# Performance work log

Measured on AMD Instinct MI355X. Metric: run time of the kernel, lower is better.

Reference implementation:

```python
import jax, jax.numpy as jnp
import numpy as np

N = 50000
E = 800000


def gcn_conv(x, row, col, dinv_sqrt, W, b, n_nodes):
    # PyG GCNConv: x' = lin(x); out[col] += norm * x'[row]; out += bias
    # norm = dinv_sqrt[row] * dinv_sqrt[col] (self-loops already in row/col)
    xw = x @ W                                  # [N, out_dim]
    norm = dinv_sqrt[row] * dinv_sqrt[col]      # [E']
    msg = xw[row] * norm[:, None]               # [E', out_dim]
    out = jax.ops.segment_sum(msg, col, num_segments=n_nodes)
    return out + b


def setup_inputs() -> dict:
    key = jax.random.key(0)
    k1, k2, k3, k4 = jax.random.split(key, 4)
    x = jax.random.normal(k1, (N, 128), dtype=jnp.float32)
    edge_index = jax.random.randint(k2, (2, E), 0, N, dtype=jnp.int64)
    W1 = jax.random.normal(k3, (128, 64), dtype=jnp.float32) * (1.0 / np.sqrt(128))
    b1 = jnp.zeros((64,), dtype=jnp.float32)
    W2 = jax.random.normal(k4, (64, 32), dtype=jnp.float32) * (1.0 / np.sqrt(64))
    b2 = jnp.zeros((32,), dtype=jnp.float32)
    return {"x": x, "edge_index": edge_index, "W1": W1, "b1": b1, "W2": W2, "b2": b2}


def reference(x, edge_index, W1, b1, W2, b2):
    n_nodes = x.shape[0]
    # add self loops (fixed size -> jit friendly)
    loops = jnp.arange(n_nodes, dtype=edge_index.dtype)
    row = jnp.concatenate([edge_index[0], loops])  # source
    col = jnp.concatenate([edge_index[1], loops])  # target
    # symmetric normalization from in-degree (all edge weights = 1)
    deg = jax.ops.segment_sum(jnp.ones_like(col, dtype=x.dtype), col, num_segments=n_nodes)
    dinv_sqrt = jnp.where(deg > 0, jax.lax.rsqrt(deg), 0.0)

    h = gcn_conv(x, row, col, dinv_sqrt, W1, b1, n_nodes)
    h = jax.nn.relu(h)
    h = gcn_conv(h, row, col, dinv_sqrt, W2, b2, n_nodes)
    return jax.nn.log_softmax(h, axis=1)
```

## Files before the change

kernel.cpp:

```cpp
#include <hip/hip_runtime.h>

#define F0 128
#define F1 64
#define F2 32
#define CPB 256
#define EPB 4096

typedef unsigned short ushort_t;
typedef unsigned int uint_t;

__device__ __forceinline__ ushort_t f2bf(float f) {
    uint_t u = __float_as_uint(f);
    return (ushort_t)((u + 0x7FFFu + ((u >> 16) & 1u)) >> 16);
}
__device__ __forceinline__ float bf2f(ushort_t u) {
    return __uint_as_float((uint_t)u << 16);
}
__device__ __forceinline__ float bflo(uint_t v) { return __uint_as_float(v << 16); }
__device__ __forceinline__ float bfhi(uint_t v) { return __uint_as_float(v & 0xFFFF0000u); }

__global__ void zero_b(int* __restrict__ bcnt) {
    bcnt[threadIdx.x] = 0;
}

__global__ __launch_bounds__(256) void bucket_count(const int* __restrict__ col,
                                                    int* __restrict__ bcnt, int E) {
    __shared__ int h[256];
    int t = threadIdx.x;
    h[t] = 0;
    __syncthreads();
    int e0 = blockIdx.x * EPB;
    int cnt = E - e0; if (cnt > EPB) cnt = EPB;
    for (int k = t; k < cnt; k += 256) atomicAdd(&h[col[e0 + k] >> 8], 1);
    __syncthreads();
    if (h[t]) atomicAdd(&bcnt[t], h[t]);
}

__global__ __launch_bounds__(256) void bucket_scan(const int* __restrict__ bcnt,
                                                   int* __restrict__ bucket_base,
                                                   int* __restrict__ cur2) {
    __shared__ int s[256];
    int t = threadIdx.x;
    int v = bcnt[t];
    s[t] = v;
    __syncthreads();
    for (int off = 1; off < 256; off <<= 1) {
        int u = (t >= off) ? s[t - off] : 0;
        __syncthreads();
        s[t] += u;
        __syncthreads();
    }
    int p = s[t] - v;
    bucket_base[t] = p;
    cur2[t] = p;
}

__global__ __launch_bounds__(256) void coarse_part(const int* __restrict__ row,
                                                   const int* __restrict__ col,
                                                   int* cur2, uint_t* __restrict__ ebuf,
                                                   int E) {
    __shared__ uint_t stage[EPB];
    __shared__ int hist[256];
    __shared__ int hbase[256];
    int t = threadIdx.x;
    int e0 = blockIdx.x * EPB;
    int cnt = E - e0; if (cnt > EPB) cnt = EPB;
    hist[t] = 0;
    __syncthreads();
    for (int k = t; k < cnt; k += 256) {
        int c = col[e0 + k], r = row[e0 + k];
        stage[k] = ((uint_t)r << 16) | (uint_t)c;
        atomicAdd(&hist[c >> 8], 1);
    }
    __syncthreads();
    int h = hist[t];
    if (h > 0) hbase[t] = atomicAdd(&cur2[t], h);
    __syncthreads();
    hist[t] = 0;
    __syncthreads();
    for (int k = t; k < cnt; k += 256) {
        uint_t p = stage[k];
        int b = (int)((p & 0xFFFFu) >> 8);
        int rk = atomicAdd(&hist[b], 1);
        ebuf[hbase[b] + rk] = p;
    }
}

__global__ __launch_bounds__(256) void fine_build(const int* __restrict__ bucket_base,
                                                  const uint_t* __restrict__ ebuf,
                                                  int* __restrict__ ptr,
                                                  float* __restrict__ dinv,
                                                  ushort_t* __restrict__ erow,
                                                  int N, int E, int nbuck) {
    __shared__ int hist[CPB];
    __shared__ int pref[CPB];
    int b = blockIdx.x;
    int cbase = b << 8;
    int t = threadIdx.x;
    int seg0 = bucket_base[b];
    int seg1 = (b + 1 < nbuck) ? bucket_base[b + 1] : E;
    hist[t] = 0;
    __syncthreads();
    for (int k = seg0 + t; k < seg1; k += 256)
        atomicAdd(&hist[ebuf[k] & 255u], 1);
    __syncthreads();
    int deg = hist[t];
    pref[t] = deg;
    __syncthreads();
    for (int off = 1; off < 256; off <<= 1) {
        int u = (t >= off) ? pref[t - off] : 0;
        __syncthreads();
        pref[t] += u;
        __syncthreads();
    }
    int base = seg0 + pref[t] - deg;
    int c = cbase + t;
    if (c < N) {
        ptr[c] = base;
        dinv[c] = rsqrtf((float)(deg + 1));
    }
    if (b == nbuck - 1 && t == 0) ptr[N] = E;
    __syncthreads();
    pref[t] = base;
    __syncthreads();
    for (int k = seg0 + t; k < seg1; k += 256) {
        uint_t p = ebuf[k];
        int pos = atomicAdd(&pref[p & 255u], 1);
        erow[pos] = (ushort_t)(p >> 16);
    }
}

__device__ __forceinline__ void fma4(float4& a, float xs, const float4& wv) {
    a.x = fmaf(xs, wv.x, a.x);
    a.y = fmaf(xs, wv.y, a.y);
    a.z = fmaf(xs, wv.z, a.z);
    a.w = fmaf(xs, wv.w, a.w);
}

__global__ __launch_bounds__(256) void gemm1(const float* __restrict__ x,
                                             const float* __restrict__ W,
                                             const float* __restrict__ dinv,
                                             ushort_t* __restrict__ xwb, int N) {
    __shared__ float Xl[64 * F0];
    __shared__ float Wl[F0 * F1];
    int tid = threadIdx.x;
    int base = blockIdx.x * 64;

    const float4* W4 = (const float4*)W;
    float4* Wl4 = (float4*)Wl;
#pragma unroll
    for (int i = 0; i < 8; ++i) Wl4[tid + 256 * i] = W4[tid + 256 * i];

    float4* Xl4 = (float4*)Xl;
#pragma unroll
    for (int i = 0; i < 8; ++i) {
        int idx = tid + 256 * i;
        int r = idx >> 5, c4 = idx & 31;
        int gr = base + r;
        float4 v = (gr < N) ? ((const float4*)x)[(size_t)gr * 32 + c4]
                            : make_float4(0.f, 0.f, 0.f, 0.f);
        Xl4[r * 32 + (c4 ^ (r >> 2))] = v;
    }
    __syncthreads();

    int tc = tid & 15, tr = tid >> 4;
    float4 acc0 = make_float4(0.f, 0.f, 0.f, 0.f);
    float4 acc1 = acc0, acc2 = acc0, acc3 = acc0;
    const float4* Wl4c = (const float4*)Wl;
    const float4* Xl4c = (const float4*)Xl;

#pragma unroll 4
    for (int kk = 0; kk < 32; ++kk) {
        float4 xv0 = Xl4c[(4 * tr + 0) * 32 + (kk ^ tr)];
        float4 xv1 = Xl4c[(4 * tr + 1) * 32 + (kk ^ tr)];
        float4 xv2 = Xl4c[(4 * tr + 2) * 32 + (kk ^ tr)];
        float4 xv3 = Xl4c[(4 * tr + 3) * 32 + (kk ^ tr)];
        float4 w0 = Wl4c[(4 * kk + 0) * 16 + tc];
        float4 w1 = Wl4c[(4 * kk + 1) * 16 + tc];
        float4 w2 = Wl4c[(4 * kk + 2) * 16 + tc];
        float4 w3 = Wl4c[(4 * kk + 3) * 16 + tc];
        fma4(acc0, xv0.x, w0); fma4(acc0, xv0.y, w1); fma4(acc0, xv0.z, w2); fma4(acc0, xv0.w, w3);
        fma4(acc1, xv1.x, w0); fma4(acc1, xv1.y, w1); fma4(acc1, xv1.z, w2); fma4(acc1, xv1.w, w3);
        fma4(acc2, xv2.x, w0); fma4(acc2, xv2.y, w1); fma4(acc2, xv2.z, w2); fma4(acc2, xv2.w, w3);
        fma4(acc3, xv3.x, w0); fma4(acc3, xv3.y, w1); fma4(acc3, xv3.z, w2); fma4(acc3, xv3.w, w3);
    }

    int gr = base + 4 * tr;
#pragma unroll
    for (int k = 0; k < 4; ++k) {
        int r = gr + k;
        if (r < N) {
            float d = dinv[r];
            float4 a = (k == 0) ? acc0 : (k == 1) ? acc1 : (k == 2) ? acc2 : acc3;
            ushort4 o = make_ushort4(f2bf(a.x * d), f2bf(a.y * d), f2bf(a.z * d), f2bf(a.w * d));
            *(ushort4*)(&xwb[(size_t)r * F1 + 4 * tc]) = o;
        }
    }
}

__global__ void agg1(const int* __restrict__ ptr, const ushort_t* __restrict__ erow,
                     const ushort_t* __restrict__ xwb, const float* __restrict__ dinv,
                     const float* __restrict__ b, ushort_t* __restrict__ h1b, int N) {
    int t = blockIdx.x * 256 + threadIdx.x;
    int i = t >> 6;
    if (i >= N) return;
    int l = t & 63, h = l >> 5, l2 = l & 31;
    const uint_t* xwb2 = (const uint_t*)xwb;

    float a0 = 0.f, a1 = 0.f;
    int e = ptr[i], end = ptr[i + 1];
    for (; e + 7 < end; e += 8) {
        int r0 = erow[e + 0 + h], r1 = erow[e + 2 + h];
        int r2 = erow[e + 4 + h], r3 = erow[e + 6 + h];
        uint_t v0 = xwb2[(size_t)r0 * 32 + l2];
        uint_t v1 = xwb2[(size_t)r1 * 32 + l2];
        uint_t v2 = xwb2[(size_t)r2 * 32 + l2];
        uint_t v3 = xwb2[(size_t)r3 * 32 + l2];
        a0 += bflo(v0); a1 += bfhi(v0);
        a0 += bflo(v1); a1 += bfhi(v1);
        a0 += bflo(v2); a1 += bfhi(v2);
        a0 += bflo(v3); a1 += bfhi(v3);
    }
    for (; e + 1 < end; e += 2) {
        int r0 = erow[e + h];
        uint_t v0 = xwb2[(size_t)r0 * 32 + l2];
        a0 += bflo(v0); a1 += bfhi(v0);
    }
    if (e < end && h == 0) {
        uint_t v0 = xwb2[(size_t)erow[e] * 32 + l2];
        a0 += bflo(v0); a1 += bfhi(v0);
    }
    a0 += __shfl_down(a0, 32, 64);
    a1 += __shfl_down(a1, 32, 64);
    if (h == 0) {
        uint_t sv = xwb2[(size_t)i * 32 + l2];
        a0 += bflo(sv); a1 += bfhi(sv);
        float d = dinv[i];
        float2 bb = ((const float2*)b)[l2];
        a0 = fmaxf(a0 * d + bb.x, 0.f);
        a1 = fmaxf(a1 * d + bb.y, 0.f);
        ((uint_t*)h1b)[(size_t)i * 32 + l2] = (uint_t)f2bf(a0) | ((uint_t)f2bf(a1) << 16);
    }
}

__global__ __launch_bounds__(256) void gemm2(const ushort_t* __restrict__ h1b,
                                             const float* __restrict__ W,
                                             const float* __restrict__ dinv,
                                             ushort_t* __restrict__ hwb, int N) {
    __shared__ float Hl[128 * F1];
    __shared__ float Wl[F1 * F2];
    int tid = threadIdx.x;
    int base = blockIdx.x * 128;

    const float4* W4 = (const float4*)W;
    float4* Wl4 = (float4*)Wl;
#pragma unroll
    for (int i = 0; i < 2; ++i) Wl4[tid + 256 * i] = W4[tid + 256 * i];

    const uint4* H4 = (const uint4*)h1b;
    float4* Hl4 = (float4*)Hl;
#pragma unroll
    for (int it = 0; it < 4; ++it) {
        int g = tid + 256 * it;
        int r = g >> 3, c8 = g & 7;
        int gr = base + r;
        uint4 v = (gr < N) ? H4[(size_t)gr * 8 + c8] : make_uint4(0, 0, 0, 0);
        float4 a, b2;
        a.x = bflo(v.x); a.y = bfhi(v.x);
        a.z = bflo(v.y); a.w = bfhi(v.y);
        b2.x = bflo(v.z); b2.y = bfhi(v.z);
        b2.z = bflo(v.w); b2.w = bfhi(v.w);
        int sw = (r >> 2) & 15;
        Hl4[r * 16 + ((2 * c8 + 0) ^ sw)] = a;
        Hl4[r * 16 + ((2 * c8 + 1) ^ sw)] = b2;
    }
    __syncthreads();

    int tc = tid & 7, tr = tid >> 3;
    float4 acc0 = make_float4(0.f, 0.f, 0.f, 0.f);
    float4 acc1 = acc0, acc2 = acc0, acc3 = acc0;
    const float4* Wl4c = (const float4*)Wl;
    const float4* Hl4c = (const float4*)Hl;

#pragma unroll 4
    for (int kk = 0; kk < 16; ++kk) {
        int sw = kk ^ (tr & 15);
        float4 xv0 = Hl4c[(4 * tr + 0) * 16 + sw];
        float4 xv1 = Hl4c[(4 * tr + 1) * 16 + sw];
        float4 xv2 = Hl4c[(4 * tr + 2) * 16 + sw];
        float4 xv3 = Hl4c[(4 * tr + 3) * 16 + sw];
        float4 w0 = Wl4c[(4 * kk + 0) * 8 + tc];
        float4 w1 = Wl4c[(4 * kk + 1) * 8 + tc];
        float4 w2 = Wl4c[(4 * kk + 2) * 8 + tc];
        float4 w3 = Wl4c[(4 * kk + 3) * 8 + tc];
        fma4(acc0, xv0.x, w0); fma4(acc0, xv0.y, w1); fma4(acc0, xv0.z, w2); fma4(acc0, xv0.w, w3);
        fma4(acc1, xv1.x, w0); fma4(acc1, xv1.y, w1); fma4(acc1, xv1.z, w2); fma4(acc1, xv1.w, w3);
        fma4(acc2, xv2.x, w0); fma4(acc2, xv2.y, w1); fma4(acc2, xv2.z, w2); fma4(acc2, xv2.w, w3);
        fma4(acc3, xv3.x, w0); fma4(acc3, xv3.y, w1); fma4(acc3, xv3.z, w2); fma4(acc3, xv3.w, w3);
    }

    int gr = base + 4 * tr;
#pragma unroll
    for (int k = 0; k < 4; ++k) {
        int r = gr + k;
        if (r < N) {
            float d = dinv[r];
            float4 a = (k == 0) ? acc0 : (k == 1) ? acc1 : (k == 2) ? acc2 : acc3;
            ushort4 o = make_ushort4(f2bf(a.x * d), f2bf(a.y * d), f2bf(a.z * d), f2bf(a.w * d));
            *(ushort4*)(&hwb[(size_t)r * F2 + 4 * tc]) = o;
        }
    }
}

__global__ void agg2_lsm(const int* __restrict__ ptr, const ushort_t* __restrict__ erow,
                         const ushort_t* __restrict__ hwb, const float* __restrict__ dinv,
                         const float* __restrict__ b, float* __restrict__ out, int N) {
    int t = blockIdx.x * 256 + threadIdx.x;
    int i = t >> 5;
    if (i >= N) return;
    int g = t & 31, h = g >> 4, l2 = g & 15;
    const uint_t* hwb2 = (const uint_t*)hwb;

    float a0 = 0.f, a1 = 0.f;
    int e = ptr[i], end = ptr[i + 1];
    for (; e + 7 < end; e += 8) {
        int r0 = erow[e + 0 + h], r1 = erow[e + 2 + h];
        int r2 = erow[e + 4 + h], r3 = erow[e + 6 + h];
        uint_t v0 = hwb2[(size_t)r0 * 16 + l2];
        uint_t v1 = hwb2[(size_t)r1 * 16 + l2];
        uint_t v2 = hwb2[(size_t)r2 * 16 + l2];
        uint_t v3 = hwb2[(size_t)r3 * 16 + l2];
        a0 += bflo(v0); a1 += bfhi(v0);
        a0 += bflo(v1); a1 += bfhi(v1);
        a0 += bflo(v2); a1 += bfhi(v2);
        a0 += bflo(v3); a1 += bfhi(v3);
    }
    for (; e + 1 < end; e += 2) {
        int r0 = erow[e + h];
        uint_t v0 = hwb2[(size_t)r0 * 16 + l2];
        a0 += bflo(v0); a1 += bfhi(v0);
    }
    if (e < end && h == 0) {
        uint_t v0 = hwb2[(size_t)erow[e] * 16 + l2];
        a0 += bflo(v0); a1 += bfhi(v0);
    }
    a0 += __shfl_down(a0, 16, 32);
    a1 += __shfl_down(a1, 16, 32);

    uint_t sv = hwb2[(size_t)i * 16 + l2];
    a0 += bflo(sv); a1 += bfhi(sv);
    float d = dinv[i];
    float2 bb = ((const float2*)b)[l2];
    a0 = a0 * d + bb.x;
    a1 = a1 * d + bb.y;

    float m = fmaxf(a0, a1);
    for (int off = 8; off; off >>= 1) m = fmaxf(m, __shfl_xor(m, off, 16));
    float s = expf(a0 - m) + expf(a1 - m);
    for (int off = 8; off; off >>= 1) s += __shfl_xor(s, off, 16);
    float ls = logf(s);
    if (h == 0)
        ((float2*)out)[(size_t)i * 16 + l2] = make_float2(a0 - m - ls, a1 - m - ls);
}

extern "C" void kernel_launch(void* const* d_in, const int* in_sizes, int n_in,
                              void* d_out, int out_size, void* d_ws, size_t ws_size,
                              hipStream_t stream) {
    const float* x  = (const float*)d_in[0];
    const int*   ei = (const int*)d_in[1];
    const float* W1 = (const float*)d_in[2];
    const float* b1 = (const float*)d_in[3];
    const float* W2 = (const float*)d_in[4];
    const float* b2 = (const float*)d_in[5];

    int N = in_sizes[0] / F0;
    int E = in_sizes[1] / 2;
    const int* row = ei;
    const int* col = ei + E;

    size_t Np = ((size_t)N + 63) & ~(size_t)63;
    size_t Ep = ((size_t)E + 63) & ~(size_t)63;
    int*      bcnt        = (int*)d_ws;
    int*      bucket_base = bcnt + 256;
    int*      cur2        = bucket_base + 256;
    int*      ptr         = cur2 + 256 + 64;
    float*    dinv        = (float*)(ptr + Np + 64);
    ushort_t* erow        = (ushort_t*)(dinv + Np);
    uint_t*   ebuf        = (uint_t*)(erow + Ep);
    ushort_t* xwb         = (ushort_t*)(ebuf + Ep);
    ushort_t* h1b         = xwb + Np * F1;
    ushort_t* hwb         = h1b + Np * F1;
    float*    out2        = (float*)d_out;

    int nbC   = (E + EPB - 1) / EPB;
    int nbuck = (N + CPB - 1) / CPB;

    zero_b<<<1, 256, 0, stream>>>(bcnt);
    bucket_count<<<nbC, 256, 0, stream>>>(col, bcnt, E);
    bucket_scan<<<1, 256, 0, stream>>>(bcnt, bucket_base, cur2);
    coarse_part<<<nbC, 256, 0, stream>>>(row, col, cur2, ebuf, E);
    fine_build<<<nbuck, 256, 0, stream>>>(bucket_base, ebuf, ptr, dinv, erow, N, E, nbuck);

    gemm1<<<(N + 63) / 64, 256, 0, stream>>>(x, W1, dinv, xwb, N);
    agg1<<<(int)(((size_t)N * 64 + 255) / 256), 256, 0, stream>>>(ptr, erow, xwb, dinv, b1, h1b, N);
    gemm2<<<(N + 127) / 128, 256, 0, stream>>>(h1b, W2, dinv, hwb, N);
    agg2_lsm<<<(int)(((size_t)N * 32 + 255) / 256), 256, 0, stream>>>(ptr, erow, hwb, dinv, b2, out2, N);
}
```

Baseline: 120.9 us.

## Replace global atomic bucket offsets with per-chunk histogram scan

Bucket counting now writes a per-chunk histogram instead of atomically accumulating global counts, so the zero-init kernel is removed. The scan kernel computes per-chunk, per-bucket start offsets serially over chunks. Coarse partitioning then reads those offsets directly, which drops its shared histogram pass and global atomics and makes the edge order deterministic. The cost is a serial loop over about 196 chunks per thread in a single-block scan kernel, plus a larger workspace.

```diff
diff --git a/kernel.cpp b/kernel.cpp
--- a/kernel.cpp
+++ b/kernel.cpp
@@ -18,13 +18,12 @@
 }
 __device__ __forceinline__ float bflo(uint_t v) { return __uint_as_float(v << 16); }
 __device__ __forceinline__ float bfhi(uint_t v) { return __uint_as_float(v & 0xFFFF0000u); }
-
-__global__ void zero_b(int* __restrict__ bcnt) {
-    bcnt[threadIdx.x] = 0;
+__device__ __forceinline__ uint_t pack2(float a, float b) {
+    return (uint_t)f2bf(a) | ((uint_t)f2bf(b) << 16);
 }
 
 __global__ __launch_bounds__(256) void bucket_count(const int* __restrict__ col,
-                                                    int* __restrict__ bcnt, int E) {
+                                                    int* __restrict__ bcnt_chunks, int E) {
     __shared__ int h[256];
     int t = threadIdx.x;
     h[t] = 0;
@@ -33,15 +32,15 @@
     int cnt = E - e0; if (cnt > EPB) cnt = EPB;
     for (int k = t; k < cnt; k += 256) atomicAdd(&h[col[e0 + k] >> 8], 1);
     __syncthreads();
-    if (h[t]) atomicAdd(&bcnt[t], h[t]);
-}
-
-__global__ __launch_bounds__(256) void bucket_scan(const int* __restrict__ bcnt,
-                                                   int* __restrict__ bucket_base,
-                                                   int* __restrict__ cur2) {
+    bcnt_chunks[blockIdx.x * 256 + t] = h[t];
+}
+
+__global__ __launch_bounds__(256) void bucket_scan(int* __restrict__ bcnt_chunks,
+                                                   int nbC, int* __restrict__ bucket_base) {
     __shared__ int s[256];
     int t = threadIdx.x;
-    int v = bcnt[t];
+    int v = 0;
+    for (int c = 0; c < nbC; ++c) v += bcnt_chunks[c * 256 + t];
     s[t] = v;
     __syncthreads();
     for (int off = 1; off < 256; off <<= 1) {
@@ -50,33 +49,32 @@
         s[t] += u;
         __syncthreads();
     }
-    int p = s[t] - v;
-    bucket_base[t] = p;
-    cur2[t] = p;
+    int run = s[t] - v;
+    bucket_base[t] = run;
+    for (int c = 0; c < nbC; ++c) {
+        int h = bcnt_chunks[c * 256 + t];
+        bcnt_chunks[c * 256 + t] = run;
+        run += h;
+    }
 }
 
 __global__ __launch_bounds__(256) void coarse_part(const int* __restrict__ row,
                                                    const int* __restrict__ col,
-                                                   int* cur2, uint_t* __restrict__ ebuf,
-                                                   int E) {
+                                                   const int* __restrict__ run_start,
+                                                   uint_t* __restrict__ ebuf, int E) {
     __shared__ uint_t stage[EPB];
     __shared__ int hist[256];
     __shared__ int hbase[256];
     int t = threadIdx.x;
     int e0 = blockIdx.x * EPB;
     int cnt = E - e0; if (cnt > EPB) cnt = EPB;
+    hbase[t] = run_start[blockIdx.x * 256 + t];
     hist[t] = 0;
     __syncthreads();
     for (int k = t; k < cnt; k += 256) {
         int c = col[e0 + k], r = row[e0 + k];
         stage[k] = ((uint_t)r << 16) | (uint_t)c;
-        atomicAdd(&hist[c >> 8], 1);
-    }
-    __syncthreads();
-    int h = hist[t];
-    if (h > 0) hbase[t] = atomicAdd(&cur2[t], h);
-    __syncthreads();
-    hist[t] = 0;
+    }
     __syncthreads();
     for (int k = t; k < cnt; k += 256) {
         uint_t p = stage[k];
@@ -239,7 +237,7 @@
         float2 bb = ((const float2*)b)[l2];
         a0 = fmaxf(a0 * d + bb.x, 0.f);
         a1 = fmaxf(a1 * d + bb.y, 0.f);
-        ((uint_t*)h1b)[(size_t)i * 32 + l2] = (uint_t)f2bf(a0) | ((uint_t)f2bf(a1) << 16);
+        ((uint_t*)h1b)[(size_t)i * 32 + l2] = pack2(a0, a1);
     }
 }
 
@@ -378,12 +376,15 @@
     const int* row = ei;
     const int* col = ei + E;
 
+    int nbC   = (E + EPB - 1) / EPB;
+    int nbuck = (N + CPB - 1) / CPB;
+
     size_t Np = ((size_t)N + 63) & ~(size_t)63;
     size_t Ep = ((size_t)E + 63) & ~(size_t)63;
-    int*      bcnt        = (int*)d_ws;
-    int*      bucket_base = bcnt + 256;
-    int*      cur2        = bucket_base + 256;
-    int*      ptr         = cur2 + 256 + 64;
+    size_t Cp = (((size_t)nbC * 256) + 63) & ~(size_t)63;
+    int*      bcnt_chunks = (int*)d_ws;
+    int*      bucket_base = bcnt_chunks + Cp;
+    int*      ptr         = bucket_base + 256 + 64;
     float*    dinv        = (float*)(ptr + Np + 64);
     ushort_t* erow        = (ushort_t*)(dinv + Np);
     uint_t*   ebuf        = (uint_t*)(erow + Ep);
@@ -392,13 +393,9 @@
     ushort_t* hwb         = h1b + Np * F1;
     float*    out2        = (float*)d_out;
 
-    int nbC   = (E + EPB - 1) / EPB;
-    int nbuck = (N + CPB - 1) / CPB;
-
-    zero_b<<<1, 256, 0, stream>>>(bcnt);
-    bucket_count<<<nbC, 256, 0, stream>>>(col, bcnt, E);
-    bucket_scan<<<1, 256, 0, stream>>>(bcnt, bucket_base, cur2);
-    coarse_part<<<nbC, 256, 0, stream>>>(row, col, cur2, ebuf, E);
+    bucket_count<<<nbC, 256, 0, stream>>>(col, bcnt_chunks, E);
+    bucket_scan<<<1, 256, 0, stream>>>(bcnt_chunks, nbC, bucket_base);
+    coarse_part<<<nbC, 256, 0, stream>>>(row, col, bcnt_chunks, ebuf, E);
     fine_build<<<nbuck, 256, 0, stream>>>(bucket_base, ebuf, ptr, dinv, erow, N, E, nbuck);
 
     gemm1<<<(N + 63) / 64, 256, 0, stream>>>(x, W1, dinv, xwb, N);
```

New measurement: 151.0 us. 1.25x slower.
